# Optimization experiments

Hardware: AMD Instinct MI355X
Metric: run time of the kernel (lower is better)

## Reference

```python
import jax, jax.numpy as jnp
import numpy as np

B, NQ, NK = 4, 384, 384
D_EQUI, D_QINV, D_KVINV = 64, 256, 256
D_MSG, D_FF, D_OUT = 64, 128, 64
IN_FEATS = 2 * D_MSG + D_EQUI  # 192


def setup_inputs() -> dict:
    key = jax.random.key(0)
    ks = jax.random.split(key, 12)
    s = lambda k, shp, fan: jax.random.normal(k, shp, jnp.float32) / np.sqrt(fan)
    return {
        "q_equi": jax.random.normal(ks[0], (B, NQ, 3, D_EQUI), jnp.float32),
        "q_inv": jax.random.normal(ks[1], (B, NQ, D_QINV), jnp.float32),
        "k_equi": jax.random.normal(ks[2], (B, NK, 3, D_EQUI), jnp.float32),
        "k_inv": jax.random.normal(ks[3], (B, NK, D_KVINV), jnp.float32),
        "Wq": s(ks[4], (D_QINV, D_MSG), D_QINV),
        "bq": jnp.zeros((D_MSG,), jnp.float32),
        "Wk": s(ks[5], (D_KVINV, D_MSG), D_KVINV),
        "bk": jnp.zeros((D_MSG,), jnp.float32),
        "W1": s(ks[6], (IN_FEATS, D_FF), IN_FEATS),
        "b1": jnp.zeros((D_FF,), jnp.float32),
        "W2": s(ks[7], (D_FF, D_OUT), D_FF),
        "b2": jnp.zeros((D_OUT,), jnp.float32),
    }


def reference(q_equi, q_inv, k_equi, k_inv, Wq, bq, Wk, bk, W1, b1, W2, b2):
    # dotprods over the 3 spatial coords, per equi-channel: [B, Nq, Nk, d_equi]
    dotprods = jnp.einsum("bqcd,bkcd->bqkd", q_equi, k_equi)
    q_msg = q_inv @ Wq + bq  # [B, Nq, d_msg]
    k_msg = k_inv @ Wk + bk  # [B, Nk, d_msg]
    b, nq, dm = q_msg.shape
    nk = k_msg.shape[1]
    # expand + concat -> [B, Nq, Nk, in_feats]
    feats = jnp.concatenate(
        [
            jnp.broadcast_to(q_msg[:, :, None, :], (b, nq, nk, dm)),
            jnp.broadcast_to(k_msg[:, None, :, :], (b, nq, nk, dm)),
            dotprods,
        ],
        axis=-1,
    )
    h = jax.nn.silu(feats @ W1 + b1)  # [B, Nq, Nk, d_ff]
    return h @ W2 + b2  # [B, Nq, Nk, d_out]
```

## Files before the change

### kernel.cpp

```cpp
#include <hip/hip_runtime.h>
#include <hip/hip_bf16.h>
#include <stdint.h>
#include <stddef.h>

#define NQ 384
#define NK 384

typedef __attribute__((ext_vector_type(4))) float float4_;
typedef __attribute__((ext_vector_type(8))) short short8;
typedef __attribute__((ext_vector_type(2))) unsigned int uint2_;

__device__ __forceinline__ short f2bf(float f) {
  union { float f; uint32_t u; } v; v.f = f;
  uint32_t u = v.u;
  uint32_t r = (u + 0x7fffu + ((u >> 16) & 1u)) >> 16;
  return (short)r;
}

__device__ __forceinline__ unsigned int pk2(float lo, float hi) {
  __hip_bfloat162 r = __float22bfloat162_rn(make_float2(lo, hi));
  union { __hip_bfloat162 b; unsigned int u; } u; u.b = r;
  return u.u;
}

__global__ __launch_bounds__(256) void prep0(
    const float* __restrict__ Wq, const float* __restrict__ Wk,
    const float* __restrict__ W1, const float* __restrict__ b1,
    const float* __restrict__ bq, const float* __restrict__ bk,
    const float* __restrict__ W2,
    float* __restrict__ Wqc, float* __restrict__ Wkc,
    float* __restrict__ c1, float* __restrict__ c2,
    short* __restrict__ W1dfrag, short* __restrict__ W2frag)
{
  int bid = blockIdx.x, t = threadIdx.x;
  if (bid < 32) {
    int side = bid >> 4;
    int r0 = (bid & 15) * 16;
    const float* W = side ? Wk : Wq;
    const float* W1s = W1 + side * 64 * 128;
    float* Wc = side ? Wkc : Wqc;
    __shared__ float sW[16][64];
    for (int j = t; j < 1024; j += 256) sW[j >> 6][j & 63] = W[(r0 + (j >> 6)) * 64 + (j & 63)];
    __syncthreads();
    int c = t & 127, rg = (t >> 7) * 8;
    float acc[8] = {0.f, 0.f, 0.f, 0.f, 0.f, 0.f, 0.f, 0.f};
    for (int k = 0; k < 64; ++k) {
      float wv = W1s[k * 128 + c];
      #pragma unroll
      for (int j = 0; j < 8; ++j) acc[j] += sW[rg + j][k] * wv;
    }
    for (int j = 0; j < 8; ++j) Wc[(r0 + rg + j) * 128 + c] = acc[j];
  } else if (bid == 32) {
    if (t < 256) {
      int c = t & 127, side = t >> 7;
      const float* bias = side ? bk : bq;
      const float* W1s = W1 + side * 64 * 128;
      float acc = side ? 0.f : b1[c];
      for (int k = 0; k < 64; ++k) acc += bias[k] * W1s[k * 128 + c];
      (side ? c2 : c1)[c] = acc;
    }
  } else {
    for (int idx = t; idx < 8192; idx += 256) {
      int fi = idx >> 9;
      int l  = (idx >> 3) & 63;
      int i  = idx & 7;
      { int n = fi >> 1, s = fi & 1;
        int d = s * 32 + ((l >> 4) << 3) + i;
        int f = n * 16 + (l & 15);
        W1dfrag[idx] = f2bf(W1[(128 + d) * 128 + f]); }
      { int n2 = fi >> 2, s2 = fi & 3;
        int k = s2 * 32 + ((l >> 4) << 3) + i;
        int o = n2 * 16 + (l & 15);
        W2frag[idx] = f2bf(W2[k * 64 + o]); }
    }
  }
}

__global__ __launch_bounds__(256) void prep1(
    const float* __restrict__ q_inv, const float* __restrict__ k_inv,
    const float* __restrict__ Wqc, const float* __restrict__ Wkc,
    const float* __restrict__ c1, const float* __restrict__ c2,
    float* __restrict__ A1, float* __restrict__ A2)
{
  int bid = blockIdx.x, t = threadIdx.x;
  int row0 = bid * 8;
  int side = row0 >= 1536;
  int r0 = row0 - side * 1536;
  const float* inv = (side ? k_inv : q_inv) + (size_t)r0 * 256;
  const float* Wc  = side ? Wkc : Wqc;
  const float* cc  = side ? c2 : c1;
  float* A = (side ? A2 : A1) + (size_t)r0 * 128;

  __shared__ float sI[8][256];
  for (int j = t; j < 2048; j += 256) sI[j >> 8][j & 255] = inv[j];
  __syncthreads();

  int c = t & 127, rg = (t >> 7) * 4;
  float acc[4] = {0.f, 0.f, 0.f, 0.f};
  for (int k = 0; k < 256; ++k) {
    float wv = Wc[k * 128 + c];
    #pragma unroll
    for (int j = 0; j < 4; ++j) acc[j] += sI[rg + j][k] * wv;
  }
  float cv = cc[c];
  #pragma unroll
  for (int j = 0; j < 4; ++j) A[(size_t)(rg + j) * 128 + c] = acc[j] + cv;
}

__global__ __launch_bounds__(512) void main_kernel(
    const float* __restrict__ q_equi, const float* __restrict__ k_equi,
    const float* __restrict__ A1, const float* __restrict__ A2,
    const short* __restrict__ W1dfrag, const short* __restrict__ W2frag,
    const float* __restrict__ b2, float* __restrict__ out)
{
  int bid0 = blockIdx.x;
  int bid = (bid0 & 7) * 288 + (bid0 >> 3);
  int b = bid / 576;
  int rem = bid - b * 576;
  int tq = rem / 24, tk = rem - (rem / 24) * 24;
  int q0 = tq * 16, k0 = tk * 16;

  __shared__ __align__(16) char smem[32768];
  float* sK = (float*)smem;

  int tid = threadIdx.x;
  int w = tid >> 6, l = tid & 63;
  int g = l >> 4, r16 = l & 15;

  const float* ksrc = k_equi + ((size_t)(b * NK + k0)) * 192;
  #pragma unroll
  for (int it = 0; it < 6; ++it) {
    int j = tid + it * 512;
    int rr = j / 192, cd = j - rr * 192;
    int c = cd >> 6, d = cd & 63;
    sK[c * 1088 + rr * 68 + d] = ksrc[j];
  }
  __syncthreads();

  const float* qrow0 = q_equi + ((size_t)(b * NQ + q0 + 2 * w)) * 192;
  short8 afrag[2][2];
  #pragma unroll
  for (int s = 0; s < 2; ++s) {
    int d0 = s * 32 + g * 8;
    float4_ kva[3], kvb[3];
    #pragma unroll
    for (int c = 0; c < 3; ++c) {
      kva[c] = *(const float4_*)&sK[c * 1088 + r16 * 68 + d0];
      kvb[c] = *(const float4_*)&sK[c * 1088 + r16 * 68 + d0 + 4];
    }
    #pragma unroll
    for (int m = 0; m < 2; ++m) {
      const float* qrow = qrow0 + m * 192;
      float da[4] = {0.f, 0.f, 0.f, 0.f};
      float db[4] = {0.f, 0.f, 0.f, 0.f};
      #pragma unroll
      for (int c = 0; c < 3; ++c) {
        float4_ qva = *(const float4_*)&qrow[c * 64 + d0];
        float4_ qvb = *(const float4_*)&qrow[c * 64 + d0 + 4];
        #pragma unroll
        for (int i = 0; i < 4; ++i) {
          da[i] += qva[i] * kva[c][i];
          db[i] += qvb[i] * kvb[c][i];
        }
      }
      union { short8 s8; unsigned int u[4]; } au;
      au.u[0] = pk2(da[0], da[1]);
      au.u[1] = pk2(da[2], da[3]);
      au.u[2] = pk2(db[0], db[1]);
      au.u[3] = pk2(db[2], db[3]);
      afrag[m][s] = au.s8;
    }
  }
  __syncthreads();

  const float* A1p = A1 + ((size_t)(b * NQ + q0 + 2 * w)) * 128;
  const float* A2p = A2 + ((size_t)(b * NK + k0)) * 128;
  float4_ acc1[2][8];
  #pragma unroll
  for (int ft = 0; ft < 8; ++ft) {
    float4_ a2v = *(const float4_*)&A2p[r16 * 128 + ft * 16 + g * 4];
    acc1[0][ft] = *(const float4_*)&A1p[ft * 16 + g * 4] + a2v;
    acc1[1][ft] = *(const float4_*)&A1p[128 + ft * 16 + g * 4] + a2v;
  }

  #pragma unroll
  for (int ft = 0; ft < 8; ++ft) {
    #pragma unroll
    for (int s = 0; s < 2; ++s) {
      short8 wf = *(const short8*)&W1dfrag[(((ft * 2 + s) * 64) + l) * 8];
      #pragma unroll
      for (int m = 0; m < 2; ++m)
        acc1[m][ft] = __builtin_amdgcn_mfma_f32_16x16x32_bf16(wf, afrag[m][s], acc1[m][ft], 0, 0, 0);
    }
  }

  char* hbase = smem + w * 4096;
  short8 hb[2][4];
  #pragma unroll
  for (int m = 0; m < 2; ++m) {
    #pragma unroll
    for (int ft = 0; ft < 8; ++ft) {
      float4_ x = acc1[m][ft];
      float y0 = x[0] / (1.f + __expf(-x[0]));
      float y1 = x[1] / (1.f + __expf(-x[1]));
      float y2 = x[2] / (1.f + __expf(-x[2]));
      float y3 = x[3] / (1.f + __expf(-x[3]));
      uint2_ pv;
      pv[0] = pk2(y0, y1);
      pv[1] = pk2(y2, y3);
      int byte = (r16 * 256 + ft * 32 + g * 8) ^ ((r16 & 7) << 4);
      *(uint2_*)(hbase + byte) = pv;
    }
    #pragma unroll
    for (int s2 = 0; s2 < 4; ++s2) {
      int byte = (r16 * 256 + s2 * 64 + g * 16) ^ ((r16 & 7) << 4);
      hb[m][s2] = *(const short8*)(hbase + byte);
    }
  }

  float4_ b2v[4];
  #pragma unroll
  for (int ot = 0; ot < 4; ++ot)
    b2v[ot] = *(const float4_*)&b2[ot * 16 + g * 4];
  float4_ acc2[2][4];
  #pragma unroll
  for (int m = 0; m < 2; ++m)
    #pragma unroll
    for (int ot = 0; ot < 4; ++ot) acc2[m][ot] = b2v[ot];
  #pragma unroll
  for (int s2 = 0; s2 < 4; ++s2) {
    #pragma unroll
    for (int ot = 0; ot < 4; ++ot) {
      short8 wf = *(const short8*)&W2frag[(((ot * 4 + s2) * 64) + l) * 8];
      #pragma unroll
      for (int m = 0; m < 2; ++m)
        acc2[m][ot] = __builtin_amdgcn_mfma_f32_16x16x32_bf16(wf, hb[m][s2], acc2[m][ot], 0, 0, 0);
    }
  }

  #pragma unroll
  for (int m = 0; m < 2; ++m) {
    float* op = out + ((size_t)(b * NQ + q0 + 2 * w + m) * NK + k0 + r16) * 64;
    #pragma unroll
    for (int ot = 0; ot < 4; ++ot)
      *(float4_*)(op + ot * 16 + g * 4) = acc2[m][ot];
  }
}

extern "C" void kernel_launch(void* const* d_in, const int* in_sizes, int n_in,
                              void* d_out, int out_size, void* d_ws, size_t ws_size,
                              hipStream_t stream) {
  (void)in_sizes; (void)n_in; (void)out_size; (void)ws_size;
  const float* q_equi = (const float*)d_in[0];
  const float* q_inv  = (const float*)d_in[1];
  const float* k_equi = (const float*)d_in[2];
  const float* k_inv  = (const float*)d_in[3];
  const float* Wq = (const float*)d_in[4];
  const float* bq = (const float*)d_in[5];
  const float* Wk = (const float*)d_in[6];
  const float* bk = (const float*)d_in[7];
  const float* W1 = (const float*)d_in[8];
  const float* b1 = (const float*)d_in[9];
  const float* W2 = (const float*)d_in[10];
  const float* b2 = (const float*)d_in[11];
  float* out = (float*)d_out;

  char* ws = (char*)d_ws;
  float* A1      = (float*)(ws);
  float* A2      = (float*)(ws + 786432);
  short* W1dfrag = (short*)(ws + 1572864);
  short* W2frag  = (short*)(ws + 1589248);
  float* Wqc     = (float*)(ws + 1605632);
  float* Wkc     = (float*)(ws + 1736704);
  float* c1      = (float*)(ws + 1867776);
  float* c2      = (float*)(ws + 1868288);

  prep0<<<34, 256, 0, stream>>>(Wq, Wk, W1, b1, bq, bk, W2, Wqc, Wkc, c1, c2, W1dfrag, W2frag);
  prep1<<<384, 256, 0, stream>>>(q_inv, k_inv, Wqc, Wkc, c1, c2, A1, A2);
  main_kernel<<<2304, 512, 0, stream>>>(q_equi, k_equi, A1, A2, W1dfrag, W2frag, b2, out);
}
```

Baseline: 261.5 us.

## Load K tile via global_load_lds with XOR swizzle, drop block remap, use rcp in SiLU

Replaces the per-element register-staged copy of the K equi tile into padded shared memory with direct 16-byte global-to-LDS loads into an XOR-swizzled row layout, and updates the shared-memory reads to match. It also removes the blockIdx remapping that interleaved blocks across groups, and swaps the SiLU division for a hardware reciprocal multiply. The aim is to cut load instruction count and staging overhead. The trade-offs are a change in L2 locality from the new block order and slightly lower SiLU precision.

Measured after the change: 253.7 us. 1.03x faster.

```diff
diff --git a/kernel.cpp b/kernel.cpp
--- a/kernel.cpp
+++ b/kernel.cpp
@@ -113,8 +113,7 @@
     const short* __restrict__ W1dfrag, const short* __restrict__ W2frag,
     const float* __restrict__ b2, float* __restrict__ out)
 {
-  int bid0 = blockIdx.x;
-  int bid = (bid0 & 7) * 288 + (bid0 >> 3);
+  int bid = blockIdx.x;
   int b = bid / 576;
   int rem = bid - b * 576;
   int tq = rem / 24, tk = rem - (rem / 24) * 24;
@@ -128,16 +127,23 @@
   int g = l >> 4, r16 = l & 15;
 
   const float* ksrc = k_equi + ((size_t)(b * NK + k0)) * 192;
-  #pragma unroll
-  for (int it = 0; it < 6; ++it) {
-    int j = tid + it * 512;
-    int rr = j / 192, cd = j - rr * 192;
-    int c = cd >> 6, d = cd & 63;
-    sK[c * 1088 + rr * 68 + d] = ksrc[j];
+  {
+    int u = tid;
+    int r = u / 48, jj = u - r * 48;
+    int j = jj ^ (r & 7);
+    __builtin_amdgcn_global_load_lds(ksrc + r * 192 + j * 4, smem + u * 16, 16, 0, 0);
+    if (tid < 256) {
+      int u2 = tid + 512;
+      int r2 = u2 / 48, jj2 = u2 - r2 * 48;
+      int j2 = jj2 ^ (r2 & 7);
+      __builtin_amdgcn_global_load_lds(ksrc + r2 * 192 + j2 * 4, smem + u2 * 16, 16, 0, 0);
+    }
   }
   __syncthreads();
 
   const float* qrow0 = q_equi + ((size_t)(b * NQ + q0 + 2 * w)) * 192;
+  const float* krow = sK + r16 * 48 * 4;
+  int x7 = r16 & 7;
   short8 afrag[2][2];
   #pragma unroll
   for (int s = 0; s < 2; ++s) {
@@ -145,8 +151,9 @@
     float4_ kva[3], kvb[3];
     #pragma unroll
     for (int c = 0; c < 3; ++c) {
-      kva[c] = *(const float4_*)&sK[c * 1088 + r16 * 68 + d0];
-      kvb[c] = *(const float4_*)&sK[c * 1088 + r16 * 68 + d0 + 4];
+      int j0 = c * 16 + s * 8 + g * 2;
+      kva[c] = *(const float4_*)&krow[((j0) ^ x7) * 4];
+      kvb[c] = *(const float4_*)&krow[((j0 + 1) ^ x7) * 4];
     }
     #pragma unroll
     for (int m = 0; m < 2; ++m) {
@@ -201,10 +208,10 @@
     #pragma unroll
     for (int ft = 0; ft < 8; ++ft) {
       float4_ x = acc1[m][ft];
-      float y0 = x[0] / (1.f + __expf(-x[0]));
-      float y1 = x[1] / (1.f + __expf(-x[1]));
-      float y2 = x[2] / (1.f + __expf(-x[2]));
-      float y3 = x[3] / (1.f + __expf(-x[3]));
+      float y0 = x[0] * __builtin_amdgcn_rcpf(1.f + __expf(-x[0]));
+      float y1 = x[1] * __builtin_amdgcn_rcpf(1.f + __expf(-x[1]));
+      float y2 = x[2] * __builtin_amdgcn_rcpf(1.f + __expf(-x[2]));
+      float y3 = x[3] * __builtin_amdgcn_rcpf(1.f + __expf(-x[3]));
       uint2_ pv;
       pv[0] = pk2(y0, y1);
       pv[1] = pk2(y2, y3);
```
